# Kernel optimization log

Measured on AMD Instinct MI355X. Metric: run time of the kernel, lower is better.

Reference implementation:

```python
import jax, jax.numpy as jnp
import numpy as np


def setup_inputs() -> dict:
    key = jax.random.key(0)
    ks = jax.random.split(key, 8)
    h = 256
    b, o, T = 64, 64, 50
    s = 1.0 / np.sqrt(h)  # torch LSTM/Linear default init scale
    return {
        "x": jax.random.normal(ks[0], (b, o, h), dtype=jnp.float32),
        "W_ih": jax.random.uniform(ks[1], (4 * h, h), jnp.float32, -s, s),
        "W_hh": jax.random.uniform(ks[2], (4 * h, h), jnp.float32, -s, s),
        "b_ih": jax.random.uniform(ks[3], (4 * h,), jnp.float32, -s, s),
        "b_hh": jax.random.uniform(ks[4], (4 * h,), jnp.float32, -s, s),
        "c0": jnp.zeros((1, h), dtype=jnp.float32),
        "W_out": jax.random.uniform(ks[5], (h, h), jnp.float32, -s, s),
        "b_out": jax.random.uniform(ks[6], (h,), jnp.float32, -s, s),
        "sequence_length": T,
    }


def reference(x, W_ih, W_hh, b_ih, b_hh, c0, W_out, b_out, sequence_length):
    b, o, f = x.shape
    B = b * o
    h0 = x.reshape(B, f)                       # initial hidden state = input
    c_init = jnp.broadcast_to(c0, (B, f))      # learned initial cell state
    # Input token is constant across time: precompute input projection once.
    x_proj = h0 @ W_ih.T + b_ih + b_hh         # (B, 4f)

    def step(carry, _):
        hp, cp = carry
        gates = x_proj + hp @ W_hh.T           # (B, 4f), torch gate order i,f,g,o
        i_g, f_g, g_g, o_g = jnp.split(gates, 4, axis=-1)
        i_g = jax.nn.sigmoid(i_g)
        f_g = jax.nn.sigmoid(f_g)
        g_g = jnp.tanh(g_g)
        o_g = jax.nn.sigmoid(o_g)
        c = f_g * cp + i_g * g_g
        hn = o_g * jnp.tanh(c)
        return (hn, c), hn

    (_, _), hs = jax.lax.scan(step, (h0, c_init), None, length=sequence_length)
    # hs: (T, B, f) -> (b, o, T, f)
    hs = hs.transpose(1, 0, 2).reshape(b, o, sequence_length, f)
    return hs @ W_out.T + b_out
```

## Files before the change

kernel.cpp:

```cpp
#include <hip/hip_runtime.h>

typedef __attribute__((ext_vector_type(8))) short short8;
typedef __attribute__((ext_vector_type(4))) float f32x4;

#define F   256
#define SH  264

__device__ __forceinline__ short f2bf(float f) {
    union { float f; unsigned u; } v; v.f = f;
    unsigned r = (v.u + 0x7fffu + ((v.u >> 16) & 1u)) >> 16;
    return (short)r;
}
__device__ __forceinline__ float bf2f(short s) {
    union { float f; unsigned u; } v; v.u = ((unsigned)(unsigned short)s) << 16;
    return v.f;
}
__device__ __forceinline__ float sigm(float x) {
    return __builtin_amdgcn_rcpf(1.f + __builtin_amdgcn_exp2f(-1.442695041f * x));
}
__device__ __forceinline__ float tanhx(float x) {
    return 1.f - 2.f * __builtin_amdgcn_rcpf(1.f + __builtin_amdgcn_exp2f(2.885390082f * x));
}
__device__ __forceinline__ f32x4 splat4(float v) {
    f32x4 r; r[0] = v; r[1] = v; r[2] = v; r[3] = v; return r;
}

__global__ void pack_kernel(const float* __restrict__ Whh, const float* __restrict__ Wih,
                            const float* __restrict__ Wout,
                            short* __restrict__ whh_p, short* __restrict__ wih_hi,
                            short* __restrict__ wih_lo, short* __restrict__ wout_p)
{
    int idx = blockIdx.x * blockDim.x + threadIdx.x;
    if (idx < 64 * 8 * 64) {
        int lane = idx & 63, kt = (idx >> 6) & 7, nt = idx >> 9;
        int n = nt * 16 + (lane & 15);
        int k = kt * 32 + (lane >> 4) * 8;
        const float* s1 = Whh + n * F + k;
        const float* s2 = Wih + n * F + k;
        #pragma unroll
        for (int j = 0; j < 8; j++) {
            whh_p[idx * 8 + j] = f2bf(s1[j]);
            float v = s2[j];
            short hi = f2bf(v);
            wih_hi[idx * 8 + j] = hi;
            wih_lo[idx * 8 + j] = f2bf(v - bf2f(hi));
        }
    } else {
        int i2 = idx - 64 * 8 * 64;
        if (i2 < 16 * 8 * 64) {
            int lane = i2 & 63, kt = (i2 >> 6) & 7, nt = i2 >> 9;
            int n = nt * 16 + (lane & 15);
            int k = kt * 32 + (lane >> 4) * 8;
            const float* s = Wout + n * F + k;
            #pragma unroll
            for (int j = 0; j < 8; j++) wout_p[i2 * 8 + j] = f2bf(s[j]);
        }
    }
}

__device__ __forceinline__ void gate_mm(f32x4 (&acc)[8][2], const short* __restrict__ Wp,
                                        const short* hb, int w, int lane)
{
    const int l15 = lane & 15, quad = lane >> 4;
    #pragma unroll
    for (int kt = 0; kt < 8; kt++) {
        short8 a0 = *(const short8*)(hb + l15 * SH + kt * 32 + quad * 8);
        short8 a1 = *(const short8*)(hb + (16 + l15) * SH + kt * 32 + quad * 8);
        #pragma unroll
        for (int i = 0; i < 8; i++) {
            int nt = (i >> 1) * 16 + 2 * w + (i & 1);
            short8 b = *(const short8*)(Wp + ((nt * 8 + kt) * 64 + lane) * 8);
            acc[i][0] = __builtin_amdgcn_mfma_f32_16x16x32_bf16(a0, b, acc[i][0], 0, 0, 0);
            acc[i][1] = __builtin_amdgcn_mfma_f32_16x16x32_bf16(a1, b, acc[i][1], 0, 0, 0);
        }
    }
}

__global__ __launch_bounds__(512, 2)
void lstm_fused(const float* __restrict__ x, const float* __restrict__ b_ih,
                const float* __restrict__ b_hh, const float* __restrict__ c0,
                const float* __restrict__ b_out,
                const short* __restrict__ whh_p, const short* __restrict__ wih_hi,
                const short* __restrict__ wih_lo, const short* __restrict__ wout_p,
                const int* __restrict__ seqlen, float* __restrict__ out)
{
    __shared__ short hbuf[32 * SH];
    const int T    = *seqlen;
    const int tid  = threadIdx.x;
    const int lane = tid & 63;
    const int w    = tid >> 6;
    const int l15  = lane & 15;
    const int quad = lane >> 4;
    const int row0 = blockIdx.x * 32;

    const int xr = tid >> 4;
    const int xc = (tid & 15) * 16;
    float xv[16];
    {
        const float* xp = x + (size_t)(row0 + xr) * F + xc;
        #pragma unroll
        for (int j = 0; j < 16; j++) xv[j] = xp[j];
    }

    f32x4 xpj[8][2];
    #pragma unroll
    for (int i = 0; i < 8; i++) { xpj[i][0] = splat4(0.f); xpj[i][1] = splat4(0.f); }

    #pragma unroll
    for (int j = 0; j < 16; j++) {
        short hi = f2bf(xv[j]);
        hbuf[xr * SH + xc + j] = f2bf(xv[j] - bf2f(hi));
    }
    __syncthreads();
    gate_mm(xpj, wih_hi, hbuf, w, lane);
    __syncthreads();
    #pragma unroll
    for (int j = 0; j < 16; j++) hbuf[xr * SH + xc + j] = f2bf(xv[j]);
    __syncthreads();
    gate_mm(xpj, wih_hi, hbuf, w, lane);
    gate_mm(xpj, wih_lo, hbuf, w, lane);

    #pragma unroll
    for (int i = 0; i < 8; i++) {
        int nt = (i >> 1) * 16 + 2 * w + (i & 1);
        float bias = b_ih[nt * 16 + l15] + b_hh[nt * 16 + l15];
        #pragma unroll
        for (int mt = 0; mt < 2; mt++)
            #pragma unroll
            for (int r = 0; r < 4; r++) xpj[i][mt][r] += bias;
    }

    float cst[2][2][4];
    float bo[2];
    #pragma unroll
    for (int s = 0; s < 2; s++) {
        float cv = c0[w * 32 + s * 16 + l15];
        bo[s]    = b_out[w * 32 + s * 16 + l15];
        #pragma unroll
        for (int mt = 0; mt < 2; mt++)
            #pragma unroll
            for (int r = 0; r < 4; r++) cst[s][mt][r] = cv;
    }

    const size_t orow = (size_t)T * F;

    for (int t = 0; t < T; t++) {
        f32x4 acc[8][2];
        #pragma unroll
        for (int i = 0; i < 8; i++) { acc[i][0] = xpj[i][0]; acc[i][1] = xpj[i][1]; }
        gate_mm(acc, whh_p, hbuf, w, lane);

        __syncthreads();

        float hv[2][2][4];
        #pragma unroll
        for (int s = 0; s < 2; s++)
          #pragma unroll
          for (int mt = 0; mt < 2; mt++)
            #pragma unroll
            for (int r = 0; r < 4; r++) {
                float ig = sigm(acc[0 + s][mt][r]);
                float fg = sigm(acc[2 + s][mt][r]);
                float gg = tanhx(acc[4 + s][mt][r]);
                float og = sigm(acc[6 + s][mt][r]);
                float c  = fg * cst[s][mt][r] + ig * gg;
                cst[s][mt][r] = c;
                float h  = og * tanhx(c);
                hv[s][mt][r] = h;
                hbuf[(mt * 16 + quad * 4 + r) * SH + w * 32 + s * 16 + l15] = f2bf(h);
            }
        __syncthreads();

        f32x4 oacc[2][2];
        #pragma unroll
        for (int s = 0; s < 2; s++) { oacc[s][0] = splat4(bo[s]); oacc[s][1] = splat4(bo[s]); }
        #pragma unroll
        for (int kt = 0; kt < 8; kt++) {
            short8 a0 = *(const short8*)(hbuf + l15 * SH + kt * 32 + quad * 8);
            short8 a1 = *(const short8*)(hbuf + (16 + l15) * SH + kt * 32 + quad * 8);
            #pragma unroll
            for (int s = 0; s < 2; s++) {
                int nt = 2 * w + s;
                short8 b = *(const short8*)(wout_p + ((nt * 8 + kt) * 64 + lane) * 8);
                oacc[s][0] = __builtin_amdgcn_mfma_f32_16x16x32_bf16(a0, b, oacc[s][0], 0, 0, 0);
                oacc[s][1] = __builtin_amdgcn_mfma_f32_16x16x32_bf16(a1, b, oacc[s][1], 0, 0, 0);
            }
        }
        float* op = out + (size_t)row0 * orow + (size_t)t * F;
        #pragma unroll
        for (int s = 0; s < 2; s++)
          #pragma unroll
          for (int mt = 0; mt < 2; mt++)
            #pragma unroll
            for (int r = 0; r < 4; r++)
                op[(size_t)(mt * 16 + quad * 4 + r) * orow + w * 32 + s * 16 + l15]
                    = oacc[s][mt][r];
    }
}

extern "C" void kernel_launch(void* const* d_in, const int* in_sizes, int n_in,
                              void* d_out, int out_size, void* d_ws, size_t ws_size,
                              hipStream_t stream)
{
    const float* x    = (const float*)d_in[0];
    const float* Wih  = (const float*)d_in[1];
    const float* Whh  = (const float*)d_in[2];
    const float* bih  = (const float*)d_in[3];
    const float* bhh  = (const float*)d_in[4];
    const float* c0   = (const float*)d_in[5];
    const float* Wout = (const float*)d_in[6];
    const float* bout = (const float*)d_in[7];
    const int* seqlen = (const int*)d_in[8];

    short* whh_p  = (short*)d_ws;
    short* wih_hi = whh_p  + 1024 * 256;
    short* wih_lo = wih_hi + 1024 * 256;
    short* wout_p = wih_lo + 1024 * 256;
    (void)ws_size; (void)in_sizes; (void)n_in; (void)out_size;

    pack_kernel<<<160, 256, 0, stream>>>(Whh, Wih, Wout, whh_p, wih_hi, wih_lo, wout_p);
    lstm_fused<<<128, 512, 0, stream>>>(x, bih, bhh, c0, bout,
                                        whh_p, wih_hi, wih_lo, wout_p,
                                        seqlen, (float*)d_out);
}
```

Before: 1.205 ms.

## Repack weights per-wave, double-buffer B loads, stage W_out in LDS, nontemporal stores

Reorders the packed W_hh/W_ih/W_out layouts so each wave reads a contiguous slab, and restructures the gate matmul to prefetch the next k-tile of weight fragments into registers while the current MFMAs run. W_out (128 KB bf16) is copied into shared memory once per block and read from LDS in the per-step output projection. Output stores become nontemporal. The aim is to hide global-memory latency of the per-step weight reads, at the cost of much more LDS per block (likely limiting occupancy to one block per CU) and higher register pressure.

```diff
diff --git a/kernel.cpp b/kernel.cpp
--- a/kernel.cpp
+++ b/kernel.cpp
@@ -35,15 +35,18 @@
         int lane = idx & 63, kt = (idx >> 6) & 7, nt = idx >> 9;
         int n = nt * 16 + (lane & 15);
         int k = kt * 32 + (lane >> 4) * 8;
+        int w = (nt & 15) >> 1;
+        int i = ((nt >> 4) << 1) | (nt & 1);
+        int dst = (((w * 8 + kt) * 8 + i) * 64 + lane) * 8;
         const float* s1 = Whh + n * F + k;
         const float* s2 = Wih + n * F + k;
         #pragma unroll
         for (int j = 0; j < 8; j++) {
-            whh_p[idx * 8 + j] = f2bf(s1[j]);
+            whh_p[dst + j] = f2bf(s1[j]);
             float v = s2[j];
             short hi = f2bf(v);
-            wih_hi[idx * 8 + j] = hi;
-            wih_lo[idx * 8 + j] = f2bf(v - bf2f(hi));
+            wih_hi[dst + j] = hi;
+            wih_lo[dst + j] = f2bf(v - bf2f(hi));
         }
     } else {
         int i2 = idx - 64 * 8 * 64;
@@ -51,27 +54,46 @@
             int lane = i2 & 63, kt = (i2 >> 6) & 7, nt = i2 >> 9;
             int n = nt * 16 + (lane & 15);
             int k = kt * 32 + (lane >> 4) * 8;
-            const float* s = Wout + n * F + k;
-            #pragma unroll
-            for (int j = 0; j < 8; j++) wout_p[i2 * 8 + j] = f2bf(s[j]);
+            int w = nt >> 1, s = nt & 1;
+            int dst = (((w * 8 + kt) * 2 + s) * 64 + lane) * 8;
+            const float* sp = Wout + n * F + k;
+            #pragma unroll
+            for (int j = 0; j < 8; j++) wout_p[dst + j] = f2bf(sp[j]);
         }
     }
 }
 
 __device__ __forceinline__ void gate_mm(f32x4 (&acc)[8][2], const short* __restrict__ Wp,
-                                        const short* hb, int w, int lane)
+                                        const short* hb, int lane)
 {
     const int l15 = lane & 15, quad = lane >> 4;
-    #pragma unroll
-    for (int kt = 0; kt < 8; kt++) {
+    const short* bp = Wp + lane * 8;
+    short8 be[8], bod[8];
+    #pragma unroll
+    for (int i = 0; i < 8; i++) be[i] = *(const short8*)(bp + i * 512);
+    #pragma unroll
+    for (int kt = 0; kt < 8; kt += 2) {
+        #pragma unroll
+        for (int i = 0; i < 8; i++)
+            bod[i] = *(const short8*)(bp + (kt + 1) * 4096 + i * 512);
         short8 a0 = *(const short8*)(hb + l15 * SH + kt * 32 + quad * 8);
         short8 a1 = *(const short8*)(hb + (16 + l15) * SH + kt * 32 + quad * 8);
         #pragma unroll
         for (int i = 0; i < 8; i++) {
-            int nt = (i >> 1) * 16 + 2 * w + (i & 1);
-            short8 b = *(const short8*)(Wp + ((nt * 8 + kt) * 64 + lane) * 8);
-            acc[i][0] = __builtin_amdgcn_mfma_f32_16x16x32_bf16(a0, b, acc[i][0], 0, 0, 0);
-            acc[i][1] = __builtin_amdgcn_mfma_f32_16x16x32_bf16(a1, b, acc[i][1], 0, 0, 0);
+            acc[i][0] = __builtin_amdgcn_mfma_f32_16x16x32_bf16(a0, be[i], acc[i][0], 0, 0, 0);
+            acc[i][1] = __builtin_amdgcn_mfma_f32_16x16x32_bf16(a1, be[i], acc[i][1], 0, 0, 0);
+        }
+        if (kt + 2 < 8) {
+            #pragma unroll
+            for (int i = 0; i < 8; i++)
+                be[i] = *(const short8*)(bp + (kt + 2) * 4096 + i * 512);
+        }
+        a0 = *(const short8*)(hb + l15 * SH + (kt + 1) * 32 + quad * 8);
+        a1 = *(const short8*)(hb + (16 + l15) * SH + (kt + 1) * 32 + quad * 8);
+        #pragma unroll
+        for (int i = 0; i < 8; i++) {
+            acc[i][0] = __builtin_amdgcn_mfma_f32_16x16x32_bf16(a0, bod[i], acc[i][0], 0, 0, 0);
+            acc[i][1] = __builtin_amdgcn_mfma_f32_16x16x32_bf16(a1, bod[i], acc[i][1], 0, 0, 0);
         }
     }
 }
@@ -85,6 +107,7 @@
                 const int* __restrict__ seqlen, float* __restrict__ out)
 {
     __shared__ short hbuf[32 * SH];
+    __shared__ short wout_lds[65536];
     const int T    = *seqlen;
     const int tid  = threadIdx.x;
     const int lane = tid & 63;
@@ -93,6 +116,18 @@
     const int quad = lane >> 4;
     const int row0 = blockIdx.x * 32;
 
+    const short* whh_w    = whh_p  + (w << 15);
+    const short* wih_hi_w = wih_hi + (w << 15);
+    const short* wih_lo_w = wih_lo + (w << 15);
+
+    {
+        const short* src = wout_p + w * 8192 + lane * 8;
+        short*       dst = wout_lds + w * 8192 + lane * 8;
+        #pragma unroll
+        for (int q = 0; q < 16; q++)
+            *(short8*)(dst + q * 512) = *(const short8*)(src + q * 512);
+    }
+
     const int xr = tid >> 4;
     const int xc = (tid & 15) * 16;
     float xv[16];
@@ -112,13 +147,13 @@
         hbuf[xr * SH + xc + j] = f2bf(xv[j] - bf2f(hi));
     }
     __syncthreads();
-    gate_mm(xpj, wih_hi, hbuf, w, lane);
+    gate_mm(xpj, wih_hi_w, hbuf, lane);
     __syncthreads();
     #pragma unroll
     for (int j = 0; j < 16; j++) hbuf[xr * SH + xc + j] = f2bf(xv[j]);
     __syncthreads();
-    gate_mm(xpj, wih_hi, hbuf, w, lane);
-    gate_mm(xpj, wih_lo, hbuf, w, lane);
+    gate_mm(xpj, wih_hi_w, hbuf, lane);
+    gate_mm(xpj, wih_lo_w, hbuf, lane);
 
     #pragma unroll
     for (int i = 0; i < 8; i++) {
@@ -143,16 +178,16 @@
     }
 
     const size_t orow = (size_t)T * F;
+    const short* wl = wout_lds + w * 8192 + lane * 8;
 
     for (int t = 0; t < T; t++) {
         f32x4 acc[8][2];
         #pragma unroll
         for (int i = 0; i < 8; i++) { acc[i][0] = xpj[i][0]; acc[i][1] = xpj[i][1]; }
-        gate_mm(acc, whh_p, hbuf, w, lane);
+        gate_mm(acc, whh_w, hbuf, lane);
 
         __syncthreads();
 
-        float hv[2][2][4];
         #pragma unroll
         for (int s = 0; s < 2; s++)
           #pragma unroll
@@ -165,9 +200,8 @@
                 float og = sigm(acc[6 + s][mt][r]);
                 float c  = fg * cst[s][mt][r] + ig * gg;
                 cst[s][mt][r] = c;
-                float h  = og * tanhx(c);
-                hv[s][mt][r] = h;
-                hbuf[(mt * 16 + quad * 4 + r) * SH + w * 32 + s * 16 + l15] = f2bf(h);
+                hbuf[(mt * 16 + quad * 4 + r) * SH + w * 32 + s * 16 + l15]
+                    = f2bf(og * tanhx(c));
             }
         __syncthreads();
 
@@ -180,8 +214,7 @@
             short8 a1 = *(const short8*)(hbuf + (16 + l15) * SH + kt * 32 + quad * 8);
             #pragma unroll
             for (int s = 0; s < 2; s++) {
-                int nt = 2 * w + s;
-                short8 b = *(const short8*)(wout_p + ((nt * 8 + kt) * 64 + lane) * 8);
+                short8 b = *(const short8*)(wl + kt * 1024 + s * 512);
                 oacc[s][0] = __builtin_amdgcn_mfma_f32_16x16x32_bf16(a0, b, oacc[s][0], 0, 0, 0);
                 oacc[s][1] = __builtin_amdgcn_mfma_f32_16x16x32_bf16(a1, b, oacc[s][1], 0, 0, 0);
             }
@@ -193,8 +226,9 @@
           for (int mt = 0; mt < 2; mt++)
             #pragma unroll
             for (int r = 0; r < 4; r++)
-                op[(size_t)(mt * 16 + quad * 4 + r) * orow + w * 32 + s * 16 + l15]
-                    = oacc[s][mt][r];
+                __builtin_nontemporal_store(
+                    oacc[s][mt][r],
+                    &op[(size_t)(mt * 16 + quad * 4 + r) * orow + w * 32 + s * 16 + l15]);
     }
 }
 
```

Result: faster. 1.018 ms (-15.6%).

## Split LSTM gate columns across workgroups with register-resident weights and global-barrier h exchange

Applied to the files above, without the earlier changes.

Each workgroup now owns a 32-column slice of the hidden state for 128 rows, so its W_hh slice stays in registers instead of being reloaded from global memory every timestep. The W_out slice is staged in LDS. Hidden states are exchanged through a double-buffered global scratch array, and the eight workgroups of a row group synchronise each step with an atomic counter spin barrier. Output stores become nontemporal. This removes the repeated weight streaming but adds a per-step inter-workgroup barrier and global round trips. It also depends on all 256 workgroups being co-resident, otherwise the spin wait can stall until its guard expires.

```diff
diff --git a/kernel.cpp b/kernel.cpp
--- a/kernel.cpp
+++ b/kernel.cpp
@@ -3,8 +3,9 @@
 typedef __attribute__((ext_vector_type(8))) short short8;
 typedef __attribute__((ext_vector_type(4))) float f32x4;
 
-#define F   256
-#define SH  264
+#define F    256
+#define SH   264
+#define ROWS 128
 
 __device__ __forceinline__ short f2bf(float f) {
     union { float f; unsigned u; } v; v.f = f;
@@ -28,22 +29,27 @@
 __global__ void pack_kernel(const float* __restrict__ Whh, const float* __restrict__ Wih,
                             const float* __restrict__ Wout,
                             short* __restrict__ whh_p, short* __restrict__ wih_hi,
-                            short* __restrict__ wih_lo, short* __restrict__ wout_p)
+                            short* __restrict__ wih_lo, short* __restrict__ wout_p,
+                            unsigned* __restrict__ ctr)
 {
     int idx = blockIdx.x * blockDim.x + threadIdx.x;
+    if (idx < 64) ctr[idx] = 0u;
     if (idx < 64 * 8 * 64) {
         int lane = idx & 63, kt = (idx >> 6) & 7, nt = idx >> 9;
         int n = nt * 16 + (lane & 15);
         int k = kt * 32 + (lane >> 4) * 8;
+        int c = (nt & 15) >> 1;
+        int i = ((nt >> 4) << 1) | (nt & 1);
+        int dst = c * 32768 + ((i * 8 + kt) * 512 + lane * 8);
         const float* s1 = Whh + n * F + k;
         const float* s2 = Wih + n * F + k;
         #pragma unroll
         for (int j = 0; j < 8; j++) {
-            whh_p[idx * 8 + j] = f2bf(s1[j]);
+            whh_p[dst + j] = f2bf(s1[j]);
             float v = s2[j];
             short hi = f2bf(v);
-            wih_hi[idx * 8 + j] = hi;
-            wih_lo[idx * 8 + j] = f2bf(v - bf2f(hi));
+            wih_hi[dst + j] = hi;
+            wih_lo[dst + j] = f2bf(v - bf2f(hi));
         }
     } else {
         int i2 = idx - 64 * 8 * 64;
@@ -51,27 +57,36 @@
             int lane = i2 & 63, kt = (i2 >> 6) & 7, nt = i2 >> 9;
             int n = nt * 16 + (lane & 15);
             int k = kt * 32 + (lane >> 4) * 8;
-            const float* s = Wout + n * F + k;
-            #pragma unroll
-            for (int j = 0; j < 8; j++) wout_p[i2 * 8 + j] = f2bf(s[j]);
-        }
-    }
-}
-
-__device__ __forceinline__ void gate_mm(f32x4 (&acc)[8][2], const short* __restrict__ Wp,
-                                        const short* hb, int w, int lane)
-{
-    const int l15 = lane & 15, quad = lane >> 4;
+            int c = nt >> 1, s = nt & 1;
+            int dst = c * 8192 + ((s * 8 + kt) * 512 + lane * 8);
+            const float* sp = Wout + n * F + k;
+            #pragma unroll
+            for (int j = 0; j < 8; j++) wout_p[dst + j] = f2bf(sp[j]);
+        }
+    }
+}
+
+__device__ __forceinline__ void load_wb(short8 (&wb)[4][8], const short* __restrict__ base,
+                                        int cw, int lane)
+{
+    #pragma unroll
+    for (int g = 0; g < 4; g++)
+        #pragma unroll
+        for (int kt = 0; kt < 8; kt++)
+            wb[g][kt] = *(const short8*)(base + (((2 * g + cw) * 8 + kt) * 512 + lane * 8));
+}
+
+__device__ __forceinline__ void mm_reg(f32x4 (&acc)[4][2], const short8 (&wb)[4][8],
+                                       const short* hb, int rw, int l15, int quad)
+{
     #pragma unroll
     for (int kt = 0; kt < 8; kt++) {
-        short8 a0 = *(const short8*)(hb + l15 * SH + kt * 32 + quad * 8);
-        short8 a1 = *(const short8*)(hb + (16 + l15) * SH + kt * 32 + quad * 8);
-        #pragma unroll
-        for (int i = 0; i < 8; i++) {
-            int nt = (i >> 1) * 16 + 2 * w + (i & 1);
-            short8 b = *(const short8*)(Wp + ((nt * 8 + kt) * 64 + lane) * 8);
-            acc[i][0] = __builtin_amdgcn_mfma_f32_16x16x32_bf16(a0, b, acc[i][0], 0, 0, 0);
-            acc[i][1] = __builtin_amdgcn_mfma_f32_16x16x32_bf16(a1, b, acc[i][1], 0, 0, 0);
+        short8 a0 = *(const short8*)(hb + (rw * 32 + l15) * SH + kt * 32 + quad * 8);
+        short8 a1 = *(const short8*)(hb + (rw * 32 + 16 + l15) * SH + kt * 32 + quad * 8);
+        #pragma unroll
+        for (int g = 0; g < 4; g++) {
+            acc[g][0] = __builtin_amdgcn_mfma_f32_16x16x32_bf16(a0, wb[g][kt], acc[g][0], 0, 0, 0);
+            acc[g][1] = __builtin_amdgcn_mfma_f32_16x16x32_bf16(a1, wb[g][kt], acc[g][1], 0, 0, 0);
         }
     }
 }
@@ -82,119 +97,163 @@
                 const float* __restrict__ b_out,
                 const short* __restrict__ whh_p, const short* __restrict__ wih_hi,
                 const short* __restrict__ wih_lo, const short* __restrict__ wout_p,
-                const int* __restrict__ seqlen, float* __restrict__ out)
-{
-    __shared__ short hbuf[32 * SH];
+                const int* __restrict__ seqlen, unsigned* __restrict__ ctr,
+                unsigned short* __restrict__ G, float* __restrict__ out)
+{
+    __shared__ short hbuf[ROWS * SH];
+    __shared__ short wlout[8192];
     const int T    = *seqlen;
     const int tid  = threadIdx.x;
     const int lane = tid & 63;
-    const int w    = tid >> 6;
+    const int wv   = tid >> 6;
+    const int rw   = wv >> 1;
+    const int cw   = wv & 1;
     const int l15  = lane & 15;
     const int quad = lane >> 4;
-    const int row0 = blockIdx.x * 32;
-
-    const int xr = tid >> 4;
-    const int xc = (tid & 15) * 16;
-    float xv[16];
-    {
-        const float* xp = x + (size_t)(row0 + xr) * F + xc;
-        #pragma unroll
-        for (int j = 0; j < 16; j++) xv[j] = xp[j];
-    }
-
-    f32x4 xpj[8][2];
-    #pragma unroll
-    for (int i = 0; i < 8; i++) { xpj[i][0] = splat4(0.f); xpj[i][1] = splat4(0.f); }
-
-    #pragma unroll
-    for (int j = 0; j < 16; j++) {
-        short hi = f2bf(xv[j]);
-        hbuf[xr * SH + xc + j] = f2bf(xv[j] - bf2f(hi));
-    }
+    const int c    = blockIdx.x & 7;
+    const int rg   = blockIdx.x >> 3;
+    const int row0 = rg * ROWS;
+
+    {
+        const short* src = wout_p + c * 8192;
+        #pragma unroll
+        for (int j = 0; j < 2; j++)
+            *(short8*)(wlout + tid * 16 + j * 8) = *(const short8*)(src + tid * 16 + j * 8);
+    }
+
+    const int xr  = tid >> 2;
+    const int xq  = (tid & 3) * 4;
+
+    f32x4 xpj[4][2];
+    #pragma unroll
+    for (int g = 0; g < 4; g++) { xpj[g][0] = splat4(0.f); xpj[g][1] = splat4(0.f); }
+
+    short8 wb[4][8];
+
+    {
+        const float* xp = x + (size_t)(row0 + xr) * F;
+        #pragma unroll
+        for (int j = 0; j < 16; j++) {
+            f32x4 v = *(const f32x4*)(xp + xq + j * 16);
+            #pragma unroll
+            for (int e = 0; e < 4; e++) {
+                short hi = f2bf(v[e]);
+                hbuf[xr * SH + xq + j * 16 + e] = f2bf(v[e] - bf2f(hi));
+            }
+        }
+    }
+    load_wb(wb, wih_hi + c * 32768, cw, lane);
     __syncthreads();
-    gate_mm(xpj, wih_hi, hbuf, w, lane);
+    mm_reg(xpj, wb, hbuf, rw, l15, quad);
     __syncthreads();
-    #pragma unroll
-    for (int j = 0; j < 16; j++) hbuf[xr * SH + xc + j] = f2bf(xv[j]);
+    {
+        const float* xp = x + (size_t)(row0 + xr) * F;
+        #pragma unroll
+        for (int j = 0; j < 16; j++) {
+            f32x4 v = *(const f32x4*)(xp + xq + j * 16);
+            #pragma unroll
+            for (int e = 0; e < 4; e++)
+                hbuf[xr * SH + xq + j * 16 + e] = f2bf(v[e]);
+        }
+    }
     __syncthreads();
-    gate_mm(xpj, wih_hi, hbuf, w, lane);
-    gate_mm(xpj, wih_lo, hbuf, w, lane);
-
-    #pragma unroll
-    for (int i = 0; i < 8; i++) {
-        int nt = (i >> 1) * 16 + 2 * w + (i & 1);
-        float bias = b_ih[nt * 16 + l15] + b_hh[nt * 16 + l15];
-        #pragma unroll
-        for (int mt = 0; mt < 2; mt++)
-            #pragma unroll
-            for (int r = 0; r < 4; r++) xpj[i][mt][r] += bias;
-    }
-
-    float cst[2][2][4];
-    float bo[2];
-    #pragma unroll
-    for (int s = 0; s < 2; s++) {
-        float cv = c0[w * 32 + s * 16 + l15];
-        bo[s]    = b_out[w * 32 + s * 16 + l15];
-        #pragma unroll
-        for (int mt = 0; mt < 2; mt++)
-            #pragma unroll
-            for (int r = 0; r < 4; r++) cst[s][mt][r] = cv;
+    mm_reg(xpj, wb, hbuf, rw, l15, quad);
+    load_wb(wb, wih_lo + c * 32768, cw, lane);
+    mm_reg(xpj, wb, hbuf, rw, l15, quad);
+    load_wb(wb, whh_p + c * 32768, cw, lane);
+
+    const int mycol = c * 32 + cw * 16 + l15;
+    #pragma unroll
+    for (int g = 0; g < 4; g++) {
+        float bias = b_ih[g * 256 + mycol] + b_hh[g * 256 + mycol];
+        #pragma unroll
+        for (int mt = 0; mt < 2; mt++)
+            #pragma unroll
+            for (int r = 0; r < 4; r++) xpj[g][mt][r] += bias;
+    }
+
+    float cst[2][4];
+    const float bo = b_out[mycol];
+    {
+        float cv = c0[mycol];
+        #pragma unroll
+        for (int mt = 0; mt < 2; mt++)
+            #pragma unroll
+            for (int r = 0; r < 4; r++) cst[mt][r] = cv;
     }
 
     const size_t orow = (size_t)T * F;
 
     for (int t = 0; t < T; t++) {
-        f32x4 acc[8][2];
-        #pragma unroll
-        for (int i = 0; i < 8; i++) { acc[i][0] = xpj[i][0]; acc[i][1] = xpj[i][1]; }
-        gate_mm(acc, whh_p, hbuf, w, lane);
+        f32x4 acc[4][2];
+        #pragma unroll
+        for (int g = 0; g < 4; g++) { acc[g][0] = xpj[g][0]; acc[g][1] = xpj[g][1]; }
+        mm_reg(acc, wb, hbuf, rw, l15, quad);
+
+        unsigned short* Gw = G + (((size_t)(t + 1) & 1) << 20);
+        #pragma unroll
+        for (int mt = 0; mt < 2; mt++)
+          #pragma unroll
+          for (int r = 0; r < 4; r++) {
+            float ig = sigm(acc[0][mt][r]);
+            float fg = sigm(acc[1][mt][r]);
+            float gg = tanhx(acc[2][mt][r]);
+            float og = sigm(acc[3][mt][r]);
+            float cn = fg * cst[mt][r] + ig * gg;
+            cst[mt][r] = cn;
+            unsigned short hb16 = (unsigned short)f2bf(og * tanhx(cn));
+            int grow = row0 + rw * 32 + mt * 16 + quad * 4 + r;
+            __hip_atomic_store(&Gw[(size_t)grow * 256 + mycol], hb16,
+                               __ATOMIC_RELAXED, __HIP_MEMORY_SCOPE_AGENT);
+          }
 
         __syncthreads();
 
-        float hv[2][2][4];
-        #pragma unroll
-        for (int s = 0; s < 2; s++)
+        if (tid == 0) {
+            __hip_atomic_fetch_add(&ctr[rg], 1u, __ATOMIC_RELEASE,
+                                   __HIP_MEMORY_SCOPE_AGENT);
+            unsigned tgt = 8u * (unsigned)(t + 1);
+            int guard = 0;
+            while (__hip_atomic_load(&ctr[rg], __ATOMIC_RELAXED,
+                                     __HIP_MEMORY_SCOPE_AGENT) < tgt
+                   && guard < (1 << 20)) {
+                __builtin_amdgcn_s_sleep(1); guard++;
+            }
+            (void)__hip_atomic_load(&ctr[rg], __ATOMIC_ACQUIRE,
+                                    __HIP_MEMORY_SCOPE_AGENT);
+        }
+        __syncthreads();
+
+        {
+            const unsigned short* gp = Gw + (size_t)(row0 + xr) * 256;
+            #pragma unroll
+            for (int j = 0; j < 16; j++) {
+                unsigned long long v = __hip_atomic_load(
+                    (const unsigned long long*)(gp + xq + j * 16),
+                    __ATOMIC_RELAXED, __HIP_MEMORY_SCOPE_AGENT);
+                *(unsigned long long*)(hbuf + xr * SH + xq + j * 16) = v;
+            }
+        }
+        __syncthreads();
+
+        f32x4 oacc[2];
+        oacc[0] = splat4(bo); oacc[1] = splat4(bo);
+        #pragma unroll
+        for (int kt = 0; kt < 8; kt++) {
+            short8 a0 = *(const short8*)(hbuf + (rw * 32 + l15) * SH + kt * 32 + quad * 8);
+            short8 a1 = *(const short8*)(hbuf + (rw * 32 + 16 + l15) * SH + kt * 32 + quad * 8);
+            short8 b  = *(const short8*)(wlout + (cw * 8 + kt) * 512 + lane * 8);
+            oacc[0] = __builtin_amdgcn_mfma_f32_16x16x32_bf16(a0, b, oacc[0], 0, 0, 0);
+            oacc[1] = __builtin_amdgcn_mfma_f32_16x16x32_bf16(a1, b, oacc[1], 0, 0, 0);
+        }
+        #pragma unroll
+        for (int mt = 0; mt < 2; mt++)
           #pragma unroll
-          for (int mt = 0; mt < 2; mt++)
-            #pragma unroll
-            for (int r = 0; r < 4; r++) {
-                float ig = sigm(acc[0 + s][mt][r]);
-                float fg = sigm(acc[2 + s][mt][r]);
-                float gg = tanhx(acc[4 + s][mt][r]);
-                float og = sigm(acc[6 + s][mt][r]);
-                float c  = fg * cst[s][mt][r] + ig * gg;
-                cst[s][mt][r] = c;
-                float h  = og * tanhx(c);
-                hv[s][mt][r] = h;
-                hbuf[(mt * 16 + quad * 4 + r) * SH + w * 32 + s * 16 + l15] = f2bf(h);
-            }
-        __syncthreads();
-
-        f32x4 oacc[2][2];
-        #pragma unroll
-        for (int s = 0; s < 2; s++) { oacc[s][0] = splat4(bo[s]); oacc[s][1] = splat4(bo[s]); }
-        #pragma unroll
-        for (int kt = 0; kt < 8; kt++) {
-            short8 a0 = *(const short8*)(hbuf + l15 * SH + kt * 32 + quad * 8);
-            short8 a1 = *(const short8*)(hbuf + (16 + l15) * SH + kt * 32 + quad * 8);
-            #pragma unroll
-            for (int s = 0; s < 2; s++) {
-                int nt = 2 * w + s;
-                short8 b = *(const short8*)(wout_p + ((nt * 8 + kt) * 64 + lane) * 8);
-                oacc[s][0] = __builtin_amdgcn_mfma_f32_16x16x32_bf16(a0, b, oacc[s][0], 0, 0, 0);
-                oacc[s][1] = __builtin_amdgcn_mfma_f32_16x16x32_bf16(a1, b, oacc[s][1], 0, 0, 0);
-            }
-        }
-        float* op = out + (size_t)row0 * orow + (size_t)t * F;
-        #pragma unroll
-        for (int s = 0; s < 2; s++)
-          #pragma unroll
-          for (int mt = 0; mt < 2; mt++)
-            #pragma unroll
-            for (int r = 0; r < 4; r++)
-                op[(size_t)(mt * 16 + quad * 4 + r) * orow + w * 32 + s * 16 + l15]
-                    = oacc[s][mt][r];
+          for (int r = 0; r < 4; r++) {
+            size_t row = (size_t)(row0 + rw * 32 + mt * 16 + quad * 4 + r);
+            __builtin_nontemporal_store(oacc[mt][r],
+                out + row * orow + (size_t)t * F + mycol);
+          }
     }
 }
 
@@ -212,14 +271,18 @@
     const float* bout = (const float*)d_in[7];
     const int* seqlen = (const int*)d_in[8];
 
-    short* whh_p  = (short*)d_ws;
-    short* wih_hi = whh_p  + 1024 * 256;
-    short* wih_lo = wih_hi + 1024 * 256;
-    short* wout_p = wih_lo + 1024 * 256;
+    char* ws = (char*)d_ws;
+    short* whh_p  = (short*)(ws);
+    short* wih_hi = (short*)(ws + 512 * 1024);
+    short* wih_lo = (short*)(ws + 1024 * 1024);
+    short* wout_p = (short*)(ws + 1536 * 1024);
+    unsigned* ctr = (unsigned*)(ws + 1664 * 1024);
+    unsigned short* G = (unsigned short*)(ws + 2048 * 1024);
     (void)ws_size; (void)in_sizes; (void)n_in; (void)out_size;
 
-    pack_kernel<<<160, 256, 0, stream>>>(Whh, Wih, Wout, whh_p, wih_hi, wih_lo, wout_p);
-    lstm_fused<<<128, 512, 0, stream>>>(x, bih, bhh, c0, bout,
+    pack_kernel<<<160, 256, 0, stream>>>(Whh, Wih, Wout, whh_p, wih_hi, wih_lo,
+                                         wout_p, ctr);
+    lstm_fused<<<256, 512, 0, stream>>>(x, bih, bhh, c0, bout,
                                         whh_p, wih_hi, wih_lo, wout_p,
-                                        seqlen, (float*)d_out);
-}
+                                        seqlen, ctr, G, (float*)d_out);
+}
```

After: 1.516 ms. 25.7% more time.
